# Kernel tuning notes

Hardware: AMD Instinct MI355X
Metric: run time of the kernel (lower is better)

The kernel has to match this reference:

```python
import math
import jax, jax.numpy as jnp
import numpy as np

NL, D, FF, V, S, BS, H = 6, 256, 1024, 1024, 48, 64, 8
NUM_CONT, NUM_CAT = 32, 16
TEMP = 0.1

def _pos_enc(L, d):
    pos = jnp.arange(L, dtype=jnp.float32)[:, None]
    div = jnp.exp(jnp.arange(0, d, 2, dtype=jnp.float32) * (-math.log(10000.0) / d))
    pe = jnp.zeros((L, d), jnp.float32)
    pe = pe.at[:, 0::2].set(jnp.sin(pos * div))
    pe = pe.at[:, 1::2].set(jnp.cos(pos * div))
    return pe

def _ln(x, w, b, eps=1e-5):
    m = x.mean(-1, keepdims=True)
    v = ((x - m) ** 2).mean(-1, keepdims=True)
    return (x - m) * jax.lax.rsqrt(v + eps) * w + b

def _mha(q_in, kv_in, wqkv, bqkv, wo, bo, mask=None):
    d = q_in.shape[-1]; dh = d // H
    wq, wk, wv = jnp.split(wqkv, 3, axis=0)
    bq, bk, bv = jnp.split(bqkv, 3)
    def proj(x, w, b):
        y = x @ w.T + b
        return y.reshape(x.shape[0], x.shape[1], H, dh).transpose(0, 2, 1, 3)
    q, k, v = proj(q_in, wq, bq), proj(kv_in, wk, bk), proj(kv_in, wv, bv)
    s = jnp.einsum('bhqd,bhkd->bhqk', q, k) * (1.0 / math.sqrt(dh))
    if mask is not None:
        s = s + mask
    a = jax.nn.softmax(s, axis=-1)
    o = jnp.einsum('bhqk,bhkd->bhqd', a, v).transpose(0, 2, 1, 3).reshape(q_in.shape)
    return o @ wo.T + bo

def setup_inputs() -> dict:
    key = jax.random.key(0)
    ks = iter(jax.random.split(key, 64))
    g = lambda shape: jax.random.normal(next(ks), shape, jnp.float32) * 0.02
    return dict(
        x_cont=jax.random.randint(next(ks), (BS, NUM_CONT), 0, V),
        x_cat=jax.random.randint(next(ks), (BS, NUM_CAT), 0, V),
        sos=g((1, 1, D)),
        emb_tab=g((S, V, D)),            # stacked per-feature embedding tables
        head_w=g((S, V, D)), head_b=jnp.zeros((S, V)),
        enc_wqkv=g((NL, 3 * D, D)), enc_bqkv=jnp.zeros((NL, 3 * D)),
        enc_wo=g((NL, D, D)), enc_bo=jnp.zeros((NL, D)),
        enc_w1=g((NL, FF, D)), enc_b1=jnp.zeros((NL, FF)),
        enc_w2=g((NL, D, FF)), enc_b2=jnp.zeros((NL, D)),
        enc_lnw=jnp.ones((NL, 2, D)), enc_lnb=jnp.zeros((NL, 2, D)),
        dec_swqkv=g((NL, 3 * D, D)), dec_sbqkv=jnp.zeros((NL, 3 * D)),
        dec_swo=g((NL, D, D)), dec_sbo=jnp.zeros((NL, D)),
        dec_cwqkv=g((NL, 3 * D, D)), dec_cbqkv=jnp.zeros((NL, 3 * D)),
        dec_cwo=g((NL, D, D)), dec_cbo=jnp.zeros((NL, D)),
        dec_w1=g((NL, FF, D)), dec_b1=jnp.zeros((NL, FF)),
        dec_w2=g((NL, D, FF)), dec_b2=jnp.zeros((NL, D)),
        dec_lnw=jnp.ones((NL, 3, D)), dec_lnb=jnp.zeros((NL, 3, D)),
        lnf_w=jnp.ones((2, D)), lnf_b=jnp.zeros((2, D)),
    )

def reference(x_cont, x_cat, sos, emb_tab, head_w, head_b,
              enc_wqkv, enc_bqkv, enc_wo, enc_bo, enc_w1, enc_b1, enc_w2, enc_b2,
              enc_lnw, enc_lnb,
              dec_swqkv, dec_sbqkv, dec_swo, dec_sbo,
              dec_cwqkv, dec_cbqkv, dec_cwo, dec_cbo,
              dec_w1, dec_b1, dec_w2, dec_b2, dec_lnw, dec_lnb, lnf_w, lnf_b):
    bs = x_cont.shape[0]
    pe = _pos_enc(S + 1, D)
    # ---- encoder over the 48 source features (post-norm, ReLU) ----
    idx = jnp.concatenate([x_cont, x_cat], axis=1)            # [bs, S]
    x = emb_tab[jnp.arange(S)[None, :], idx] + pe[None, :S]   # [bs, S, D]
    for l in range(NL):
        a = _mha(x, x, enc_wqkv[l], enc_bqkv[l], enc_wo[l], enc_bo[l])
        x = _ln(x + a, enc_lnw[l, 0], enc_lnb[l, 0])
        f = jax.nn.relu(x @ enc_w1[l].T + enc_b1[l]) @ enc_w2[l].T + enc_b2[l]
        x = _ln(x + f, enc_lnw[l, 1], enc_lnb[l, 1])
    memory = _ln(x, lnf_w[0], lnf_b[0])

    Lt = S + 1
    causal = jnp.triu(jnp.full((Lt, Lt), -1e9, jnp.float32), k=1)

    def decode(tgt):  # full decoder stack recomputed every step (no KV cache)
        y = tgt
        for l in range(NL):
            a = _mha(y, y, dec_swqkv[l], dec_sbqkv[l], dec_swo[l], dec_sbo[l], causal)
            y = _ln(y + a, dec_lnw[l, 0], dec_lnb[l, 0])
            c = _mha(y, memory, dec_cwqkv[l], dec_cbqkv[l], dec_cwo[l], dec_cbo[l])
            y = _ln(y + c, dec_lnw[l, 1], dec_lnb[l, 1])
            f = jax.nn.relu(y @ dec_w1[l].T + dec_b1[l]) @ dec_w2[l].T + dec_b2[l]
            y = _ln(y + f, dec_lnw[l, 2], dec_lnb[l, 2])
        return _ln(y, lnf_w[1], lnf_b[1])

    buf0 = jnp.zeros((bs, Lt, D), jnp.float32).at[:, 0].set(sos[0, 0])
    step_keys = jax.random.split(jax.random.key(42), S)

    def step(buf, xs):
        i, k, hw, hb, et = xs
        h = decode(buf + pe[None])          # [bs, Lt, D]
        hi = jnp.take(h, i, axis=1)          # last generated position [bs, D]
        logits = hi @ hw.T + hb              # [bs, V]
        choice = jax.random.categorical(k, logits / TEMP)
        buf = buf.at[:, i + 1].set(et[choice])
        return buf, (choice, logits)

    _, (choices, logits_all) = jax.lax.scan(
        step, buf0, (jnp.arange(S), step_keys, head_w, head_b, emb_tab))
    s_cont = choices[:NUM_CONT].T            # [bs, num_cont]
    s_cat = choices[NUM_CONT:].T             # [bs, num_cat]
    return s_cont, s_cat, logits_all
```

## Files before the change

### kernel.cpp

```cpp
#include <hip/hip_runtime.h>
#include <math.h>

#define JAX_PARTITIONABLE 1


static constexpr int SWQKVT  = 0;
static constexpr int SWOT    = SWQKVT + 6*256*768;
static constexpr int CWQT    = SWOT   + 6*256*256;
static constexpr int CWOT    = CWQT   + 6*256*256;
static constexpr int DW1T    = CWOT   + 6*256*256;
static constexpr int DW2T    = DW1T   + 6*256*1024;
static constexpr int WT_END  = DW2T   + 6*1024*256;
static constexpr int CKT_OFF = WT_END;
static constexpr int CV_OFF  = CKT_OFF + 6*64*48*256;
static constexpr int SKT_OFF = CV_OFF  + 6*64*48*256;
static constexpr int SV_OFF  = SKT_OFF + 6*64*48*256;
static constexpr int WS_END  = SV_OFF  + 6*64*48*256;
static constexpr int X_OFF    = 0;
static constexpr int MEM_OFF  = X_OFF + 3072*256;
static constexpr int QKV_OFF  = SKT_OFF;
static constexpr int AO_OFF   = QKV_OFF + 3072*768;
static constexpr int RES1_OFF = AO_OFF + 3072*256;
static constexpr int X1_OFF   = RES1_OFF + 3072*256;
static constexpr int HB_OFF   = SV_OFF;
static constexpr int RES2_OFF = HB_OFF + 3072*1024;
static constexpr int PCK_OFF  = SKT_OFF;
static constexpr int SSYNC_OFF = WS_END;

struct GParams {
  const int   *xc, *xct;
  const float *sos, *emb, *hw, *hb;
  const float *ewqkv, *ebqkv, *ewo, *ebo, *ew1, *eb1, *ew2, *eb2, *elnw, *elnb;
  const float *swqkv, *sbqkv, *swo, *sbo;
  const float *cwqkv, *cbqkv, *cwo, *cbo;
  const float *dw1, *db1, *dw2, *db2, *dlnw, *dlnb, *lnfw, *lnfb;
  float *out;
  float *ws;
};

__device__ unsigned g_cntA = 0, g_genA = 0;

static __device__ __forceinline__ void gbar(unsigned* cnt, unsigned* gen, unsigned nb) {
  __syncthreads();
  if (threadIdx.x == 0) {
    __threadfence();
    unsigned g = __hip_atomic_load(gen, __ATOMIC_RELAXED, __HIP_MEMORY_SCOPE_AGENT);
    unsigned prev = __hip_atomic_fetch_add(cnt, 1u, __ATOMIC_ACQ_REL, __HIP_MEMORY_SCOPE_AGENT);
    if (prev == nb - 1u) {
      __hip_atomic_store(cnt, 0u, __ATOMIC_RELAXED, __HIP_MEMORY_SCOPE_AGENT);
      __threadfence();
      __hip_atomic_store(gen, g + 1u, __ATOMIC_RELEASE, __HIP_MEMORY_SCOPE_AGENT);
    } else {
      while (__hip_atomic_load(gen, __ATOMIC_ACQUIRE, __HIP_MEMORY_SCOPE_AGENT) == g)
        __builtin_amdgcn_s_sleep(1);
      __threadfence();
    }
  }
  __syncthreads();
}

static __device__ __forceinline__ void cohort_sync(unsigned* slot) {
  __syncthreads();
  if (threadIdx.x == 0) {
    __hip_atomic_fetch_add(slot, 1u, __ATOMIC_RELAXED, __HIP_MEMORY_SCOPE_AGENT);
    for (int it = 0; it < 64; ++it) {
      if (__hip_atomic_load(slot, __ATOMIC_RELAXED, __HIP_MEMORY_SCOPE_AGENT) >= 8u) break;
      __builtin_amdgcn_s_sleep(1);
    }
  }
  __syncthreads();
}

static __device__ __forceinline__ void tf2x32(unsigned k0, unsigned k1, unsigned& x0, unsigned& x1) {
  unsigned ks2 = k0 ^ k1 ^ 0x1BD11BDAu;
  x0 += k0; x1 += k1;
#define TF_R(r) { x0 += x1; x1 = (x1 << r) | (x1 >> (32 - r)); x1 ^= x0; }
  TF_R(13) TF_R(15) TF_R(26) TF_R(6)   x0 += k1;  x1 += ks2 + 1u;
  TF_R(17) TF_R(29) TF_R(16) TF_R(24)  x0 += ks2; x1 += k0  + 2u;
  TF_R(13) TF_R(15) TF_R(26) TF_R(6)   x0 += k0;  x1 += k1  + 3u;
  TF_R(17) TF_R(29) TF_R(16) TF_R(24)  x0 += k1;  x1 += ks2 + 4u;
  TF_R(13) TF_R(15) TF_R(26) TF_R(6)   x0 += ks2; x1 += k0  + 5u;
#undef TF_R
}

static __device__ __forceinline__ void step_key(int i, unsigned& k0, unsigned& k1) {
#if JAX_PARTITIONABLE
  unsigned x0 = 0u, x1 = (unsigned)i;
  tf2x32(0u, 42u, x0, x1);
  k0 = x0; k1 = x1;
#else
  unsigned w[2];
  for (int wi = 0; wi < 2; wi++) {
    unsigned o = (unsigned)(2*i + wi), x0, x1;
    if (o < 48u) { x0 = o; x1 = 48u + o; tf2x32(0u, 42u, x0, x1); w[wi] = x0; }
    else         { x0 = o - 48u; x1 = o; tf2x32(0u, 42u, x0, x1); w[wi] = x1; }
  }
  k0 = w[0]; k1 = w[1];
#endif
}

static __device__ __forceinline__ unsigned gumbel_bits(unsigned k0, unsigned k1, int b, int v) {
#if JAX_PARTITIONABLE
  unsigned x0 = 0u, x1 = (unsigned)(b*1024 + v);
  tf2x32(k0, k1, x0, x1);
  return x0 ^ x1;
#else
  unsigned jj = (unsigned)((b & 31)*1024 + v);
  unsigned x0 = jj, x1 = 32768u + jj;
  tf2x32(k0, k1, x0, x1);
  return (b < 32) ? x0 : x1;
#endif
}

static __device__ __forceinline__ float pe_val(int p, int c) {
  const float KC = (float)(-9.210340371976184 / 256.0);
  int j = c >> 1;
  float dv = expf((float)(2*j) * KC);
  float a = (float)p * dv;
  return (c & 1) ? cosf(a) : sinf(a);
}

static __device__ __forceinline__ void wave_ln_row(float* row, const float* lw, const float* lb) {
  const int lane = threadIdx.x & 63;
  float x0 = row[lane], x1 = row[lane+64], x2 = row[lane+128], x3 = row[lane+192];
  float s = (x0 + x1) + (x2 + x3);
#pragma unroll
  for (int m = 1; m < 64; m <<= 1) s += __shfl_xor(s, m);
  float mean = s * 0.00390625f;
  float d0 = x0-mean, d1 = x1-mean, d2 = x2-mean, d3 = x3-mean;
  float q = (d0*d0 + d1*d1) + (d2*d2 + d3*d3);
#pragma unroll
  for (int m = 1; m < 64; m <<= 1) q += __shfl_xor(q, m);
  float rs = 1.0f / sqrtf(q * 0.00390625f + 1e-5f);
  row[lane]     = d0*rs*lw[lane]     + lb[lane];
  row[lane+64]  = d1*rs*lw[lane+64]  + lb[lane+64];
  row[lane+128] = d2*rs*lw[lane+128] + lb[lane+128];
  row[lane+192] = d3*rs*lw[lane+192] + lb[lane+192];
}

template<int C, int KS, int K>
static __device__ void matvec_t(const float* __restrict__ wt, const float* __restrict__ x,
                                float* __restrict__ part) {
  const int t = threadIdx.x;
  constexpr int O4 = C/4;
  constexpr int KC = K/KS;
  constexpr int BT = (KC < 32) ? KC : 32;
  if (t < O4*KS) {
    const int kc = t / O4, o4 = t - kc*O4;
    const int k0 = kc*KC;
    float4 acc = {0.f,0.f,0.f,0.f};
    const float* wp = wt + k0*C + o4*4;
    for (int kb = 0; kb < KC; kb += BT) {
      float4 w[BT];
#pragma unroll
      for (int j = 0; j < BT; j++) w[j] = *(const float4*)(wp + (kb + j)*C);
      __builtin_amdgcn_sched_barrier(0);
#pragma unroll
      for (int j4 = 0; j4 < BT/4; j4++) {
        float4 xv = *(const float4*)(x + k0 + kb + j4*4);
        float4 a0 = w[j4*4+0], a1 = w[j4*4+1], a2 = w[j4*4+2], a3 = w[j4*4+3];
        acc.x += xv.x*a0.x; acc.y += xv.x*a0.y; acc.z += xv.x*a0.z; acc.w += xv.x*a0.w;
        acc.x += xv.y*a1.x; acc.y += xv.y*a1.y; acc.z += xv.y*a1.z; acc.w += xv.y*a1.w;
        acc.x += xv.z*a2.x; acc.y += xv.z*a2.y; acc.z += xv.z*a2.z; acc.w += xv.z*a2.w;
        acc.x += xv.w*a3.x; acc.y += xv.w*a3.y; acc.z += xv.w*a3.z; acc.w += xv.w*a3.w;
      }
    }
    *(float4*)(part + kc*C + o4*4) = acc;
  }
  __syncthreads();
}

static __device__ void gemm_stage(const float* __restrict__ A, const float* __restrict__ W,
                                  const float* __restrict__ bias, const float* __restrict__ res,
                                  float* __restrict__ out, int R, int C, int K, int relu,
                                  float* sA) {
  const int t = threadIdx.x;
  const bool act = (t < 256);
  const int lane = t & 63, wv = (t >> 6) & 3;
  const int ntc = C >> 6;
  const int ntiles = (R >> 5) * ntc;
  for (int tile = blockIdx.x; tile < ntiles; tile += gridDim.x) {
    const int tr = tile / ntc, tc = tile - tr*ntc;
    const int r0 = tr << 5;
    const int c  = (tc << 6) + lane;
    float acc[8] = {0,0,0,0,0,0,0,0};
    for (int kc = 0; kc < K; kc += 256) {
      __syncthreads();
      if (act) {
#pragma unroll
        for (int u = 0; u < 8; u++) {
          int idx = u*256 + t;
          int rr = idx >> 6, cc = idx & 63;
          ((float4*)sA)[idx] = *(const float4*)(A + (r0+rr)*K + kc + cc*4);
        }
      }
      __syncthreads();
      if (act) {
        const float* wr = W + c*K + kc;
        for (int k = 0; k < 256; k += 4) {
          float4 w4 = *(const float4*)(wr + k);
#pragma unroll
          for (int r = 0; r < 8; r++) {
            float4 a4 = *(const float4*)(sA + (wv*8 + r)*256 + k);
            acc[r] += a4.x*w4.x; acc[r] += a4.y*w4.y; acc[r] += a4.z*w4.z; acc[r] += a4.w*w4.w;
          }
        }
      }
    }
    if (act) {
      float bb = bias ? bias[c] : 0.0f;
#pragma unroll
      for (int r = 0; r < 8; r++) {
        int row = r0 + wv*8 + r;
        float v = acc[r] + bb;
        if (relu) v = fmaxf(v, 0.0f);
        if (res)  v += res[row*C + c];
        out[row*C + c] = v;
      }
    }
  }
}

static __device__ void ln_stage(const float* in, const float* lw, const float* lb,
                                float* out, int R) {
  const int lane = threadIdx.x & 63;
  int gw = blockIdx.x*8 + (threadIdx.x >> 6);
  for (int row = gw; row < R; row += gridDim.x*8) {
    const float* ir = in + row*256;
    float x0 = ir[lane], x1 = ir[lane+64], x2 = ir[lane+128], x3 = ir[lane+192];
    float s = (x0 + x1) + (x2 + x3);
#pragma unroll
    for (int m = 1; m < 64; m <<= 1) s += __shfl_xor(s, m);
    float mean = s * 0.00390625f;
    float d0 = x0-mean, d1 = x1-mean, d2 = x2-mean, d3 = x3-mean;
    float q = (d0*d0 + d1*d1) + (d2*d2 + d3*d3);
#pragma unroll
    for (int m = 1; m < 64; m <<= 1) q += __shfl_xor(q, m);
    float rs = 1.0f / sqrtf(q * 0.00390625f + 1e-5f);
    float* orow = out + row*256;
    orow[lane]     = d0*rs*lw[lane]     + lb[lane];
    orow[lane+64]  = d1*rs*lw[lane+64]  + lb[lane+64];
    orow[lane+128] = d2*rs*lw[lane+128] + lb[lane+128];
    orow[lane+192] = d3*rs*lw[lane+192] + lb[lane+192];
  }
}

static __device__ void attn_core(const float* qd, const float* kb, const float* vb,
                                 int krstride, int kstride, int nk,
                                 float* sc, float* red, float* ao) {
  const int t = threadIdx.x;
  const int r = t >> 5, p0 = t & 31;
  const bool act = (t < 256);
  if (act) {
#pragma unroll
    for (int pass = 0; pass < 2; pass++) {
      int p = pass*32 + p0;
      if (p < nk) {
        const float4* k4 = (const float4*)(kb + r*krstride + p*kstride);
        const float4* q4 = (const float4*)(qd + r*32);
        float a = 0.0f;
#pragma unroll
        for (int d4 = 0; d4 < 8; d4++) {
          float4 kv = k4[d4], qv = q4[d4];
          a += qv.x*kv.x; a += qv.y*kv.y; a += qv.z*kv.z; a += qv.w*kv.w;
        }
        sc[r*48 + p] = a * 0.17677669529663687f;
      }
    }
  }
  __syncthreads();
  if (t < 8) {
    float m = sc[t*48];
    for (int p = 1; p < nk; p++) m = fmaxf(m, sc[t*48 + p]);
    red[t] = m;
  }
  __syncthreads();
  if (act) {
#pragma unroll
    for (int pass = 0; pass < 2; pass++) {
      int p = pass*32 + p0;
      if (p < nk) sc[r*48 + p] = expf(sc[r*48 + p] - red[r]);
    }
  }
  __syncthreads();
  if (t < 8) {
    float s = 0.0f;
    for (int p = 0; p < nk; p++) s += sc[t*48 + p];
    red[8 + t] = s;
  }
  __syncthreads();
  if (act) {
#pragma unroll
    for (int pass = 0; pass < 2; pass++) {
      int p = pass*32 + p0;
      if (p < nk) sc[r*48 + p] = sc[r*48 + p] / red[8 + r];
    }
  }
  __syncthreads();
  if (act) {
    const int d2 = t & 31;
    const float* vr = vb + r*krstride + d2;
    float a = 0.0f;
    for (int p = 0; p < nk; p++) a += sc[r*48 + p] * vr[p*kstride];
    ao[r*32 + d2] = a;
  }
  __syncthreads();
}

static __device__ void enc_attn_stage(const float* QKV, float* AO, float* sm) {
  const int t = threadIdx.x;
  const bool act = (t < 256);
  float* qd  = sm;
  float* sc  = sm + 256;
  float* ao  = sm + 640;
  float* red = sm + 896;
  for (int pi = blockIdx.x; pi < 512; pi += gridDim.x) {
    int b = pi >> 3, h = pi & 7;
    const float* Qb = QKV + b*48*768 + h*32;
    const float* Kb = QKV + b*48*768 + 256 + h*32;
    const float* Vb = QKV + b*48*768 + 512 + h*32;
    for (int qg = 0; qg < 6; qg++) {
      if (act) { int r = t >> 5, d2 = t & 31; qd[r*32 + d2] = Qb[(qg*8 + r)*768 + d2]; }
      __syncthreads();
      attn_core(qd, Kb, Vb, 0, 768, 48, sc, red, ao);
      if (act) { int r = t >> 5, d2 = t & 31; AO[(b*48 + qg*8 + r)*256 + h*32 + d2] = ao[r*32 + d2]; }
      __syncthreads();
    }
  }
}

static __device__ void attn_dec(const float* qd, const float* kt, const float* v,
                                int nk, float* sc, float* red, float* ao) {
  const int t = threadIdx.x;
  const int r = t >> 5, p0 = t & 31;
  const bool act = (t < 256);
  if (act) {
    const float4* q4 = (const float4*)(qd + r*32);
#pragma unroll
    for (int pass = 0; pass < 2; pass++) {
      int p = pass*32 + p0;
      if (p < nk) {
        const float* kb = kt + r*1536 + p*4;
        float4 kv[8];
#pragma unroll
        for (int j = 0; j < 8; j++) kv[j] = *(const float4*)(kb + j*192);
        __builtin_amdgcn_sched_barrier(0);
        float a = 0.0f;
#pragma unroll
        for (int j = 0; j < 8; j++) {
          float4 qv = q4[j];
          a += qv.x*kv[j].x; a += qv.y*kv[j].y; a += qv.z*kv[j].z; a += qv.w*kv[j].w;
        }
        sc[r*48 + p] = a * 0.17677669529663687f;
      }
    }
  }
  __syncthreads();
  if (t < 8) {
    const float* scr = sc + t*48;
    float m = scr[0];
    int p = 1;
    for (; p + 8 <= nk; p += 8) {
      float s0=scr[p],s1=scr[p+1],s2=scr[p+2],s3=scr[p+3],
            s4=scr[p+4],s5=scr[p+5],s6=scr[p+6],s7=scr[p+7];
      m=fmaxf(m,s0); m=fmaxf(m,s1); m=fmaxf(m,s2); m=fmaxf(m,s3);
      m=fmaxf(m,s4); m=fmaxf(m,s5); m=fmaxf(m,s6); m=fmaxf(m,s7);
    }
    for (; p < nk; p++) m = fmaxf(m, scr[p]);
    red[t] = m;
  }
  __syncthreads();
  if (act) {
#pragma unroll
    for (int pass = 0; pass < 2; pass++) {
      int p = pass*32 + p0;
      if (p < nk) sc[r*48 + p] = expf(sc[r*48 + p] - red[r]);
    }
  }
  __syncthreads();
  if (t < 8) {
    const float* scr = sc + t*48;
    float s = 0.0f;
    int p = 0;
    for (; p + 8 <= nk; p += 8) {
      float s0=scr[p],s1=scr[p+1],s2=scr[p+2],s3=scr[p+3],
            s4=scr[p+4],s5=scr[p+5],s6=scr[p+6],s7=scr[p+7];
      s+=s0; s+=s1; s+=s2; s+=s3; s+=s4; s+=s5; s+=s6; s+=s7;
    }
    for (; p < nk; p++) s += scr[p];
    red[8 + t] = s;
  }
  __syncthreads();
  if (act) {
#pragma unroll
    for (int pass = 0; pass < 2; pass++) {
      int p = pass*32 + p0;
      if (p < nk) sc[r*48 + p] = sc[r*48 + p] / red[8 + r];
    }
  }
  __syncthreads();
  if (act) {
    const int d2 = t & 31;
    const float* vr = v + r*32 + d2;
    float a = 0.0f;
    int p = 0;
    for (; p + 8 <= nk; p += 8) {
      float vv[8], ss[8];
#pragma unroll
      for (int j = 0; j < 8; j++) vv[j] = vr[(p+j)*256];
#pragma unroll
      for (int j = 0; j < 8; j++) ss[j] = sc[r*48 + p + j];
      __builtin_amdgcn_sched_barrier(0);
#pragma unroll
      for (int j = 0; j < 8; j++) a += ss[j] * vv[j];
    }
    for (; p < nk; p++) a += sc[r*48 + p] * vr[p*256];
    ao[r*32 + d2] = a;
  }
  __syncthreads();
}

__global__ void __launch_bounds__(512)
genrev7_kernel(GParams P) {
  __shared__ float sm[8448];
  float* ws = P.ws;
  const int wg = blockIdx.x;
  const int t  = threadIdx.x;

  if (t < 256) {
    for (int rr = 0; rr < 12; rr++) {
      int row = wg*12 + rr;
      int b = row / 48, s = row % 48;
      int tok = (s < 32) ? P.xc[b*32 + s] : P.xct[b*16 + (s - 32)];
      ws[X_OFF + row*256 + t] = P.emb[(s*1024 + tok)*256 + t] + pe_val(s, t);
    }
  }
  gbar(&g_cntA, &g_genA, 256);

  float* Xp = ws + X_OFF;
  for (int l = 0; l < 6; l++) {
    gemm_stage(Xp, P.ewqkv + l*768*256, P.ebqkv + l*768, nullptr, ws + QKV_OFF, 3072, 768, 256, 0, sm);
    gbar(&g_cntA, &g_genA, 256);
    enc_attn_stage(ws + QKV_OFF, ws + AO_OFF, sm);
    gbar(&g_cntA, &g_genA, 256);
    gemm_stage(ws + AO_OFF, P.ewo + l*256*256, P.ebo + l*256, Xp, ws + RES1_OFF, 3072, 256, 256, 0, sm);
    gbar(&g_cntA, &g_genA, 256);
    ln_stage(ws + RES1_OFF, P.elnw + (l*2 + 0)*256, P.elnb + (l*2 + 0)*256, ws + X1_OFF, 3072);
    gbar(&g_cntA, &g_genA, 256);
    gemm_stage(ws + X1_OFF, P.ew1 + l*1024*256, P.eb1 + l*1024, nullptr, ws + HB_OFF, 3072, 1024, 256, 1, sm);
    gbar(&g_cntA, &g_genA, 256);
    gemm_stage(ws + HB_OFF, P.ew2 + l*256*1024, P.eb2 + l*256, ws + X1_OFF, ws + RES2_OFF, 3072, 256, 1024, 0, sm);
    gbar(&g_cntA, &g_genA, 256);
    ln_stage(ws + RES2_OFF, P.elnw + (l*2 + 1)*256, P.elnb + (l*2 + 1)*256, Xp, 3072);
    gbar(&g_cntA, &g_genA, 256);
  }
  ln_stage(Xp, P.lnfw, P.lnfb, ws + MEM_OFF, 3072);
  gbar(&g_cntA, &g_genA, 256);
  for (int l = 0; l < 6; l++) {
    gemm_stage(ws + MEM_OFF, P.cwqkv + (l*768 + 256)*256, P.cbqkv + l*768 + 256, nullptr,
               ws + PCK_OFF + l*786432, 3072, 256, 256, 0, sm);
    gemm_stage(ws + MEM_OFF, P.cwqkv + (l*768 + 512)*256, P.cbqkv + l*768 + 512, nullptr,
               ws + CV_OFF + l*786432, 3072, 256, 256, 0, sm);
  }
  gbar(&g_cntA, &g_genA, 256);

  {
    const int gt = wg*512 + t;
    const int GT = 256*512;
    for (int idx = gt; idx < 6*256*768; idx += GT) {
      int l = idx / 196608, r = idx - l*196608;
      int k = r / 768, o = r - k*768;
      ws[SWQKVT + idx] = P.swqkv[(l*768 + o)*256 + k];
    }
    for (int idx = gt; idx < 6*65536; idx += GT) {
      int l = idx >> 16, r = idx & 65535, k = r >> 8, o = r & 255;
      ws[SWOT + idx] = P.swo[(l*256 + o)*256 + k];
    }
    for (int idx = gt; idx < 6*65536; idx += GT) {
      int l = idx >> 16, r = idx & 65535, k = r >> 8, o = r & 255;
      ws[CWQT + idx] = P.cwqkv[(l*768 + o)*256 + k];
    }
    for (int idx = gt; idx < 6*65536; idx += GT) {
      int l = idx >> 16, r = idx & 65535, k = r >> 8, o = r & 255;
      ws[CWOT + idx] = P.cwo[(l*256 + o)*256 + k];
    }
    for (int idx = gt; idx < 6*262144; idx += GT) {
      int l = idx >> 18, r = idx & 262143, k = r >> 10, o = r & 1023;
      ws[DW1T + idx] = P.dw1[(l*1024 + o)*256 + k];
    }
    for (int idx = gt; idx < 6*262144; idx += GT) {
      int l = idx >> 18, r = idx & 262143, k = r >> 8, o = r & 255;
      ws[DW2T + idx] = P.dw2[(l*256 + o)*1024 + k];
    }
    for (int idx = gt; idx < 6*64*48*256; idx += GT) {
      int l = idx / 786432, r = idx - l*786432;
      int b = r / 12288, q = r - b*12288;
      int d4 = q / 192, s2 = q - d4*192;
      int p = s2 >> 2, c = s2 & 3;
      ws[CKT_OFF + idx] = ws[PCK_OFF + l*786432 + (b*48 + p)*256 + d4*4 + c];
    }
    unsigned* ssync = (unsigned*)(ws + SSYNC_OFF);
    for (int idx = gt; idx < 3072; idx += GT)
      __hip_atomic_store(&ssync[idx], 0u, __ATOMIC_RELAXED, __HIP_MEMORY_SCOPE_AGENT);
  }
  gbar(&g_cntA, &g_genA, 256);

  if (wg >= 64) return;
  const int b = wg;
  const int grp = wg & 7;
  unsigned* ssync = (unsigned*)(ws + SSYNC_OFF);

  float* cur  = sm;
  float* qv   = sm + 256;
  float* av   = sm + 512;
  float* y1   = sm + 768;
  float* y2   = sm + 1024;
  float* hbf  = sm + 1280;
  float* sc   = sm + 2304;
  float* red  = sm + 2688;
  float* y0   = sm + 2720;
  float* bvv  = sm + 2976;
  int*   bii  = (int*)(sm + 3232);
  float* part = sm + 3488;

  if (t < 256) y0[t] = P.sos[t] + pe_val(0, t);
  __syncthreads();

  for (int i = 0; i < 48; i++) {
    if (t < 256) cur[t] = y0[t];
    __syncthreads();
    for (int l = 0; l < 6; l++) {
      cohort_sync(ssync + (i*7 + l)*8 + grp);
      const int skt = SKT_OFF + l*786432 + b*12288;
      const int sv  = SV_OFF  + l*786432 + b*12288;
      const int ckt = CKT_OFF + l*786432 + b*12288;
      const int cv  = CV_OFF  + l*786432 + b*12288;
      matvec_t<768,2,256>(ws + SWQKVT + l*196608, cur, part);
      for (int o = t; o < 768; o += 512) {
        float v = part[o] + part[768 + o] + P.sbqkv[l*768 + o];
        if (o < 256)      qv[o] = v;
        else if (o < 512) { int d = o - 256; ws[skt + (d>>2)*192 + i*4 + (d&3)] = v; }
        else              ws[sv + i*256 + (o - 512)] = v;
      }
      __syncthreads();
      attn_dec(qv, ws + skt, ws + sv, i + 1, sc, red, av);
      matvec_t<256,8,256>(ws + SWOT + l*65536, av, part);
      if (t < 256) {
        float s = part[t];
#pragma unroll
        for (int kc = 1; kc < 8; kc++) s += part[kc*256 + t];
        y1[t] = cur[t] + (s + P.sbo[l*256 + t]);
      }
      __syncthreads();
      if (t < 64) wave_ln_row(y1, P.dlnw + (l*3 + 0)*256, P.dlnb + (l*3 + 0)*256);
      __syncthreads();
      matvec_t<256,8,256>(ws + CWQT + l*65536, y1, part);
      if (t < 256) {
        float s = part[t];
#pragma unroll
        for (int kc = 1; kc < 8; kc++) s += part[kc*256 + t];
        qv[t] = s + P.cbqkv[l*768 + t];
      }
      __syncthreads();
      attn_dec(qv, ws + ckt, ws + cv, 48, sc, red, av);
      matvec_t<256,8,256>(ws + CWOT + l*65536, av, part);
      if (t < 256) {
        float s = part[t];
#pragma unroll
        for (int kc = 1; kc < 8; kc++) s += part[kc*256 + t];
        y2[t] = y1[t] + (s + P.cbo[l*256 + t]);
      }
      __syncthreads();
      if (t < 64) wave_ln_row(y2, P.dlnw + (l*3 + 1)*256, P.dlnb + (l*3 + 1)*256);
      __syncthreads();
      matvec_t<1024,2,256>(ws + DW1T + l*262144, y2, part);
      for (int o = t; o < 1024; o += 512)
        hbf[o] = fmaxf(part[o] + part[1024 + o] + P.db1[l*1024 + o], 0.0f);
      __syncthreads();
      matvec_t<256,8,1024>(ws + DW2T + l*262144, hbf, part);
      if (t < 256) {
        float s = part[t];
#pragma unroll
        for (int kc = 1; kc < 8; kc++) s += part[kc*256 + t];
        cur[t] = y2[t] + (s + P.db2[l*256 + t]);
      }
      __syncthreads();
      if (t < 64) wave_ln_row(cur, P.dlnw + (l*3 + 2)*256, P.dlnb + (l*3 + 2)*256);
      __syncthreads();
    }
    if (t < 64) wave_ln_row(cur, P.lnfw + 256, P.lnfb + 256);
    __syncthreads();
    cohort_sync(ssync + (i*7 + 6)*8 + grp);
    {
      const int wv = t >> 6, lane = t & 63;
      const float4 x4 = *(const float4*)(cur + lane*4);
      for (int base = 0; base < 1024; base += 64) {
        float4 wl[8];
#pragma unroll
        for (int u = 0; u < 4; u++) {
          int o = base + u*16 + wv;
          wl[u*2]   = *(const float4*)(P.hw + (size_t)(i*1024 + o)*256 + lane*4);
          wl[u*2+1] = *(const float4*)(P.hw + (size_t)(i*1024 + o + 8)*256 + lane*4);
        }
        __builtin_amdgcn_sched_barrier(0);
#pragma unroll
        for (int u = 0; u < 4; u++) {
          int o = base + u*16 + wv, o2 = o + 8;
          float4 wa = wl[u*2], wb = wl[u*2+1];
          float sa = wa.x*x4.x; sa += wa.y*x4.y; sa += wa.z*x4.z; sa += wa.w*x4.w;
          float sb = wb.x*x4.x; sb += wb.y*x4.y; sb += wb.z*x4.z; sb += wb.w*x4.w;
#pragma unroll
          for (int m = 1; m < 64; m <<= 1) { sa += __shfl_xor(sa, m); sb += __shfl_xor(sb, m); }
          if (lane == 0) {
            hbf[o]  = sa + P.hb[i*1024 + o];
            hbf[o2] = sb + P.hb[i*1024 + o2];
          }
        }
      }
    }
    __syncthreads();
    for (int o = t; o < 1024; o += 512)
      P.out[3072 + i*65536 + b*1024 + o] = hbf[o];
    __syncthreads();
    unsigned k0, k1;
    step_key(i, k0, k1);
    if (t < 256) {
      float bestv = -INFINITY; int besti = 0;
#pragma unroll
      for (int e = 0; e < 4; e++) {
        int v = t*4 + e;
        unsigned bits = gumbel_bits(k0, k1, b, v);
        float f = __uint_as_float((bits >> 9) | 0x3f800000u);
        float u = fmaxf(f - 1.0f, 1.17549435e-38f);
        float g = -logf(-logf(u));
        float z = g + hbf[v] / 0.1f;
        if (z > bestv) { bestv = z; besti = v; }
      }
      bvv[t] = bestv; bii[t] = besti;
    }
    __syncthreads();
    for (int s = 128; s > 0; s >>= 1) {
      if (t < s) {
        float ov = bvv[t+s]; int oi = bii[t+s];
        if (ov > bvv[t] || (ov == bvv[t] && oi < bii[t])) { bvv[t] = ov; bii[t] = oi; }
      }
      __syncthreads();
    }
    const int ch = bii[0];
    if (t == 0) {
      if (i < 32) P.out[b*32 + i] = (float)ch;
      else        P.out[2048 + b*16 + (i - 32)] = (float)ch;
    }
    if (t < 256) y0[t] = P.emb[(i*1024 + ch)*256 + t] + pe_val(i + 1, t);
    __syncthreads();
  }
}

extern "C" void kernel_launch(void* const* d_in, const int* in_sizes, int n_in,
                              void* d_out, int out_size, void* d_ws, size_t ws_size,
                              hipStream_t stream) {
  (void)in_sizes; (void)n_in; (void)out_size; (void)ws_size;
  GParams p;
  p.xc    = (const int*)  d_in[0];
  p.xct   = (const int*)  d_in[1];
  p.sos   = (const float*)d_in[2];
  p.emb   = (const float*)d_in[3];
  p.hw    = (const float*)d_in[4];
  p.hb    = (const float*)d_in[5];
  p.ewqkv = (const float*)d_in[6];
  p.ebqkv = (const float*)d_in[7];
  p.ewo   = (const float*)d_in[8];
  p.ebo   = (const float*)d_in[9];
  p.ew1   = (const float*)d_in[10];
  p.eb1   = (const float*)d_in[11];
  p.ew2   = (const float*)d_in[12];
  p.eb2   = (const float*)d_in[13];
  p.elnw  = (const float*)d_in[14];
  p.elnb  = (const float*)d_in[15];
  p.swqkv = (const float*)d_in[16];
  p.sbqkv = (const float*)d_in[17];
  p.swo   = (const float*)d_in[18];
  p.sbo   = (const float*)d_in[19];
  p.cwqkv = (const float*)d_in[20];
  p.cbqkv = (const float*)d_in[21];
  p.cwo   = (const float*)d_in[22];
  p.cbo   = (const float*)d_in[23];
  p.dw1   = (const float*)d_in[24];
  p.db1   = (const float*)d_in[25];
  p.dw2   = (const float*)d_in[26];
  p.db2   = (const float*)d_in[27];
  p.dlnw  = (const float*)d_in[28];
  p.dlnb  = (const float*)d_in[29];
  p.lnfw  = (const float*)d_in[30];
  p.lnfb  = (const float*)d_in[31];
  p.out   = (float*)d_out;
  p.ws    = (float*)d_ws;
  hipLaunchKernelGGL(genrev7_kernel, dim3(256), dim3(512), 0, stream, p);
}
```

Baseline: 20.28 ms.

## Prefetch next-stage weights and KV cache into L2 using idle threads

```diff
diff --git a/kernel.cpp b/kernel.cpp
--- a/kernel.cpp
+++ b/kernel.cpp
@@ -71,6 +71,44 @@
   __syncthreads();
 }
 
+static __device__ __forceinline__ unsigned pf_slice(const float* base, int nfloats, int q,
+                                                    int tid, int nthr) {
+  const unsigned* p = (const unsigned*)base;
+  const int lines = nfloats >> 5;
+  unsigned acc = 0;
+  for (int j = q + (tid << 3); j < lines; j += (nthr << 3))
+    acc ^= p[(size_t)j << 5];
+  return acc;
+}
+static __device__ __forceinline__ unsigned pf_full(const float* base, int nfloats,
+                                                   int tid, int nthr) {
+  const unsigned* p = (const unsigned*)base;
+  const int lines = nfloats >> 5;
+  unsigned acc = 0;
+  for (int j = tid; j < lines; j += nthr)
+    acc ^= p[(size_t)j << 5];
+  return acc;
+}
+
+struct PF {
+  const float* r0; int n0;
+  const float* r1; int n1;
+  const float* r2; int n2;
+  const float* rp; int np;
+  const float* rp2; int np2;
+  int q;
+};
+
+static __device__ __forceinline__ void do_pf(const PF* pf, int tid, int nthr) {
+  unsigned acc = 0;
+  if (pf->r0)  acc ^= pf_slice(pf->r0,  pf->n0,  pf->q, tid, nthr);
+  if (pf->r1)  acc ^= pf_slice(pf->r1,  pf->n1,  pf->q, tid, nthr);
+  if (pf->r2)  acc ^= pf_slice(pf->r2,  pf->n2,  pf->q, tid, nthr);
+  if (pf->rp)  acc ^= pf_full (pf->rp,  pf->np,  tid, nthr);
+  if (pf->rp2) acc ^= pf_full (pf->rp2, pf->np2, tid, nthr);
+  asm volatile("" :: "v"(acc));
+}
+
 static __device__ __forceinline__ void tf2x32(unsigned k0, unsigned k1, unsigned& x0, unsigned& x1) {
   unsigned ks2 = k0 ^ k1 ^ 0x1BD11BDAu;
   x0 += k0; x1 += k1;
@@ -140,7 +178,7 @@
 
 template<int C, int KS, int K>
 static __device__ void matvec_t(const float* __restrict__ wt, const float* __restrict__ x,
-                                float* __restrict__ part) {
+                                float* __restrict__ part, const PF* pf = nullptr) {
   const int t = threadIdx.x;
   constexpr int O4 = C/4;
   constexpr int KC = K/KS;
@@ -166,6 +204,8 @@
       }
     }
     *(float4*)(part + kc*C + o4*4) = acc;
+  } else if (pf) {
+    do_pf(pf, t - O4*KS, 512 - O4*KS);
   }
   __syncthreads();
 }
@@ -330,7 +370,7 @@
 }
 
 static __device__ void attn_dec(const float* qd, const float* kt, const float* v,
-                                int nk, float* sc, float* red, float* ao) {
+                                int nk, float* sc, float* red, float* ao, const PF* pf) {
   const int t = threadIdx.x;
   const int r = t >> 5, p0 = t & 31;
   const bool act = (t < 256);
@@ -354,6 +394,8 @@
         sc[r*48 + p] = a * 0.17677669529663687f;
       }
     }
+  } else if (pf) {
+    do_pf(pf, t - 256, 256);
   }
   __syncthreads();
   if (t < 8) {
@@ -420,8 +462,8 @@
   __syncthreads();
 }
 
-__global__ void __launch_bounds__(512)
-genrev7_kernel(GParams P) {
+__global__ void __launch_bounds__(512, 2)
+genrev8_kernel(GParams P) {
   __shared__ float sm[8448];
   float* ws = P.ws;
   const int wg = blockIdx.x;
@@ -508,6 +550,7 @@
   if (wg >= 64) return;
   const int b = wg;
   const int grp = wg & 7;
+  const int qsl = wg >> 3;
   unsigned* ssync = (unsigned*)(ws + SSYNC_OFF);
 
   float* cur  = sm;
@@ -535,7 +578,25 @@
       const int sv  = SV_OFF  + l*786432 + b*12288;
       const int ckt = CKT_OFF + l*786432 + b*12288;
       const int cv  = CV_OFF  + l*786432 + b*12288;
-      matvec_t<768,2,256>(ws + SWQKVT + l*196608, cur, part);
+      PF pfqkv;
+      pfqkv.r0 = nullptr; pfqkv.r1 = nullptr; pfqkv.r2 = nullptr;
+      pfqkv.rp = ws + skt; pfqkv.np = 12288;
+      pfqkv.rp2 = ws + sv; pfqkv.np2 = 12288;
+      pfqkv.q = qsl;
+      PF pfself;
+      pfself.r0 = ws + SWOT + l*65536; pfself.n0 = 65536;
+      pfself.r1 = ws + CWQT + l*65536; pfself.n1 = 65536;
+      pfself.r2 = ws + CWOT + l*65536; pfself.n2 = 65536;
+      pfself.rp = ws + ckt; pfself.np = 12288;
+      pfself.rp2 = ws + cv; pfself.np2 = 12288;
+      pfself.q = qsl;
+      PF pfcross;
+      pfcross.r0 = ws + DW1T + l*262144; pfcross.n0 = 262144;
+      pfcross.r1 = ws + DW2T + l*262144; pfcross.n1 = 262144;
+      pfcross.r2 = ws + SWQKVT + ((l == 5) ? 0 : (l+1))*196608; pfcross.n2 = 196608;
+      pfcross.rp = nullptr; pfcross.rp2 = nullptr;
+      pfcross.q = qsl;
+      matvec_t<768,2,256>(ws + SWQKVT + l*196608, cur, part, &pfqkv);
       for (int o = t; o < 768; o += 512) {
         float v = part[o] + part[768 + o] + P.sbqkv[l*768 + o];
         if (o < 256)      qv[o] = v;
@@ -543,7 +604,7 @@
         else              ws[sv + i*256 + (o - 512)] = v;
       }
       __syncthreads();
-      attn_dec(qv, ws + skt, ws + sv, i + 1, sc, red, av);
+      attn_dec(qv, ws + skt, ws + sv, i + 1, sc, red, av, &pfself);
       matvec_t<256,8,256>(ws + SWOT + l*65536, av, part);
       if (t < 256) {
         float s = part[t];
@@ -562,7 +623,7 @@
         qv[t] = s + P.cbqkv[l*768 + t];
       }
       __syncthreads();
-      attn_dec(qv, ws + ckt, ws + cv, 48, sc, red, av);
+      attn_dec(qv, ws + ckt, ws + cv, 48, sc, red, av, &pfcross);
       matvec_t<256,8,256>(ws + CWOT + l*65536, av, part);
       if (t < 256) {
         float s = part[t];
@@ -588,7 +649,12 @@
       if (t < 64) wave_ln_row(cur, P.dlnw + (l*3 + 2)*256, P.dlnb + (l*3 + 2)*256);
       __syncthreads();
     }
-    if (t < 64) wave_ln_row(cur, P.lnfw + 256, P.lnfb + 256);
+    if (t < 64) {
+      wave_ln_row(cur, P.lnfw + 256, P.lnfb + 256);
+    } else {
+      unsigned acc = pf_slice(P.hw + (size_t)i*262144, 262144, qsl, t - 64, 448);
+      asm volatile("" :: "v"(acc));
+    }
     __syncthreads();
     cohort_sync(ssync + (i*7 + 6)*8 + grp);
     {
@@ -637,6 +703,9 @@
         if (z > bestv) { bestv = z; besti = v; }
       }
       bvv[t] = bestv; bii[t] = besti;
+    } else {
+      unsigned acc = pf_slice(ws + SWQKVT, 196608, qsl, t - 256, 256);
+      asm volatile("" :: "v"(acc));
     }
     __syncthreads();
     for (int s = 128; s > 0; s >>= 1) {
@@ -695,5 +764,5 @@
   p.lnfb  = (const float*)d_in[31];
   p.out   = (float*)d_out;
   p.ws    = (float*)d_ws;
-  hipLaunchKernelGGL(genrev7_kernel, dim3(256), dim3(512), 0, stream, p);
-}
+  hipLaunchKernelGGL(genrev8_kernel, dim3(256), dim3(512), 0, stream, p);
+}
```

Measured after the change: 21.14 ms. 4.2% more time.
